# Kernel tuning notes

Measured on AMD Instinct MI355X. Metric: run time of the kernel, lower is better.

Reference implementation:

```python
import jax, jax.numpy as jnp
import numpy as np

N_JOINTS = 24

def _rodrigues(r):
    # r: [B, J, 3] axis-angle -> [B, J, 3, 3] rotation matrices
    theta = jnp.clip(jnp.linalg.norm(r, axis=-1, keepdims=True), 1e-6)  # [B,J,1]
    rh = r / theta
    z = jnp.zeros_like(rh[..., :1])
    # skew-symmetric matrix m
    m = jnp.stack([
        jnp.concatenate([z, -rh[..., 2:3], rh[..., 1:2]], -1),
        jnp.concatenate([rh[..., 2:3], z, -rh[..., 0:1]], -1),
        jnp.concatenate([-rh[..., 1:2], rh[..., 0:1], z], -1),
    ], axis=-2)  # [B,J,3,3]
    rrT = rh[..., :, None] * rh[..., None, :]  # outer product [B,J,3,3]
    cos = jnp.cos(theta)[..., None]
    sin = jnp.sin(theta)[..., None]
    eye = jnp.eye(3, dtype=r.dtype)
    return cos * eye + (1.0 - cos) * rrT + sin * m

def _with_zeros(Rm, t):
    # Rm: [B,3,3], t: [B,3] -> [B,4,4] homogeneous transform
    B = Rm.shape[0]
    top = jnp.concatenate([Rm, t[:, :, None]], axis=-1)  # [B,3,4]
    bot = jnp.broadcast_to(jnp.array([0.0, 0.0, 0.0, 1.0], Rm.dtype), (B, 1, 4))
    return jnp.concatenate([top, bot], axis=1)

def _keypoints(v, idx):
    # v: [B,N,3], idx: [G,K] vertex-index groups -> [B,G,3] via (max+min)/2
    g = v[:, idx]  # [B,G,K,3] irregular gather
    return (g.max(axis=2) + g.min(axis=2)) * 0.5

def setup_inputs() -> dict:
    key = jax.random.key(0)
    ks = jax.random.split(key, 8)
    B, N, P, K = 64, 40000, 100, 128
    beta = jax.random.normal(ks[0], (B, P), jnp.float32)
    pose = jax.random.normal(ks[1], (B, N_JOINTS * 3), jnp.float32) * 0.3
    trans = jax.random.normal(ks[2], (B, 3), jnp.float32)
    shapedirs = jax.random.normal(ks[3], (P, 3 * N), jnp.float32) * 0.01
    v_template = jax.random.normal(ks[4], (N, 3), jnp.float32)
    w = jax.random.uniform(ks[5], (N, N_JOINTS), jnp.float32)
    weights = w / w.sum(axis=1, keepdims=True)  # LBS weights sum to 1
    reorder_index = jnp.arange(N_JOINTS, dtype=jnp.int64 if jax.config.jax_enable_x64 else jnp.int32)
    # kinematic tree: parent[i] < i (binary-tree shape stands in for the rabbit skeleton)
    parent = jnp.concatenate([jnp.zeros(1, jnp.int32), (jnp.arange(1, N_JOINTS, dtype=jnp.int32) - 1) // 2])
    joint_idx = jax.random.randint(ks[6], (N_JOINTS - 1, K), 0, N)
    add_idx = jax.random.randint(ks[7], (7, K), 0, N)
    return {"beta": beta, "pose": pose, "trans": trans, "shapedirs": shapedirs,
            "v_template": v_template, "weights": weights, "reorder_index": reorder_index,
            "parent": parent, "joint_idx": joint_idx, "add_idx": add_idx}

def reference(beta, pose, trans, shapedirs, v_template, weights,
              reorder_index, parent, joint_idx, add_idx):
    B = beta.shape[0]
    pose = pose.reshape(B, N_JOINTS, 3)[:, reorder_index]
    # blend shapes: v_shaped = beta @ shapedirs + template
    v_posed = (beta @ shapedirs + v_template.reshape(-1)).reshape(B, -1, 3)  # [B,N,3]
    # joints from vertex-group (max+min)/2, root is zero
    J = jnp.concatenate([jnp.zeros((B, 1, 3), beta.dtype), _keypoints(v_posed, joint_idx)], axis=1)  # [B,24,3]
    R = _rodrigues(pose)  # [B,24,3,3]
    # forward kinematics along the tree (fixed 24-joint loop)
    par = np.asarray(jax.device_get(parent))
    G = [_with_zeros(R[:, 0], J[:, 0])]
    for i in range(1, N_JOINTS):
        p = int(par[i])
        G_loc = _with_zeros(R[:, i], J[:, i] - J[:, p])
        G.append(jnp.matmul(G[p], G_loc))
    G = jnp.stack(G, axis=1)  # [B,24,4,4]
    # remove rest-pose joint locations (pack subtraction only touches last column)
    Jh = jnp.concatenate([J, jnp.zeros((B, N_JOINTS, 1), beta.dtype)], axis=-1)[..., None]  # [B,24,4,1]
    t_corr = jnp.matmul(G, Jh)  # [B,24,4,1]
    G1 = jnp.concatenate([G[..., :3], G[..., 3:4] - t_corr], axis=-1)
    # LBS skinning: per-vertex blended transform
    T = jnp.einsum('nk,bkij->bnij', weights, G1)  # [B,N,4,4]
    vh = jnp.concatenate([v_posed, jnp.ones((B, v_posed.shape[1], 1), beta.dtype)], axis=-1)  # [B,N,4]
    posed = jnp.einsum('bnij,bnj->bni', T, vh)[..., :3] + trans[:, None, :]  # [B,N,3]
    skeleton = jnp.concatenate([
        jnp.zeros((B, 1, 3), beta.dtype),
        _keypoints(posed, joint_idx),
        _keypoints(posed, add_idx),
    ], axis=1)  # [B,31,3]
    return posed, skeleton
```

## Files before the change

### kernel.cpp

```cpp
#include <hip/hip_runtime.h>
#include <math.h>

#define B   64
#define NV  40000
#define P   100
#define KG  128
#define NJ  24
#define TV  16
#define NSK 31
#define NSUB (KG / TV)

typedef __attribute__((ext_vector_type(8))) short bf16x8;
typedef __attribute__((ext_vector_type(4))) float f32x4;

__device__ __forceinline__ unsigned short rne_bf16(float f) {
  unsigned u = __float_as_uint(f);
  u = (u + 0x7FFFu + ((u >> 16) & 1u)) >> 16;
  return (unsigned short)u;
}

__global__ __launch_bounds__(256)
void k_jpart(const float* __restrict__ beta,
             const float* __restrict__ sd,
             const float* __restrict__ vt,
             const int*   __restrict__ joint_idx,
             float*       __restrict__ pmn,
             float*       __restrict__ pmx) {
  const int j = blockIdx.x;
  const int s = blockIdx.y;
  const int t = threadIdx.x;
  const int lane = t & 63, wv = t >> 6;
  const int l15 = lane & 15, qd = lane >> 4;

  __shared__ __align__(16) unsigned short beta_s[64 * 136];
  __shared__ __align__(16) unsigned short sdT_s[48 * 136];
  __shared__ float vt_s[48];
  __shared__ int   idx_s[TV];
  float* pos_s = (float*)beta_s;

  if (t < TV) idx_s[t] = joint_idx[j * KG + s * TV + t];
  __syncthreads();

  for (int e = t; e < 64 * 36; e += 256) {
    const int m = e / 36, pp = P + e % 36;
    beta_s[m * 136 + pp] = 0;
  }
  for (int e = t; e < 64 * P; e += 256) {
    const int m = e / P, p = e % P;
    beta_s[m * 136 + p] = rne_bf16(beta[e]);
  }
  for (int task = t; task < 768; task += 256) {
    const int n = task % 48, kg = task / 48;
    const size_t colbase = (size_t)idx_s[n / 3] * 3 + (n % 3);
    unsigned pk[4];
#pragma unroll
    for (int h = 0; h < 4; ++h) {
      const int k0 = kg * 8 + 2 * h;
      float f0 = 0.0f, f1 = 0.0f;
      if (k0 < P)     f0 = sd[(size_t)k0 * (3 * NV) + colbase];
      if (k0 + 1 < P) f1 = sd[(size_t)(k0 + 1) * (3 * NV) + colbase];
      pk[h] = (unsigned)rne_bf16(f0) | ((unsigned)rne_bf16(f1) << 16);
    }
    *(uint4*)&sdT_s[n * 136 + kg * 8] = make_uint4(pk[0], pk[1], pk[2], pk[3]);
  }
  if (t < 48) vt_s[t] = vt[(size_t)idx_s[t / 3] * 3 + (t % 3)];
  __syncthreads();

  bf16x8 af[4];
#pragma unroll
  for (int ks = 0; ks < 4; ++ks)
    af[ks] = *(const bf16x8*)&beta_s[(wv * 16 + l15) * 136 + ks * 32 + qd * 8];
  f32x4 acc[3];
#pragma unroll
  for (int nt = 0; nt < 3; ++nt) acc[nt] = (f32x4){0.f, 0.f, 0.f, 0.f};
#pragma unroll
  for (int ks = 0; ks < 4; ++ks) {
#pragma unroll
    for (int nt = 0; nt < 3; ++nt) {
      const bf16x8 bf = *(const bf16x8*)&sdT_s[(nt * 16 + l15) * 136 + ks * 32 + qd * 8];
      acc[nt] = __builtin_amdgcn_mfma_f32_16x16x32_bf16(af[ks], bf, acc[nt], 0, 0, 0);
    }
  }
  float vtv[3];
#pragma unroll
  for (int nt = 0; nt < 3; ++nt) vtv[nt] = vt_s[nt * 16 + l15];
  __syncthreads();

#pragma unroll
  for (int nt = 0; nt < 3; ++nt) {
    const int n = nt * 16 + l15;
    const int v = n / 3, c = n - 3 * v;
#pragma unroll
    for (int r = 0; r < 4; ++r) {
      const int m = wv * 16 + qd * 4 + r;
      pos_s[m * 68 + v * 4 + c] = acc[nt][r] + vtv[nt];
    }
  }
  __syncthreads();

  if (t < 192) {
    const int b = t / 3, c = t % 3;
    float lo = 1e30f, hi = -1e30f;
#pragma unroll
    for (int v = 0; v < TV; ++v) {
      const float val = pos_s[b * 68 + v * 4 + c];
      lo = fminf(lo, val); hi = fmaxf(hi, val);
    }
    pmn[((j * NSUB + s) * B + b) * 3 + c] = lo;
    pmx[((j * NSUB + s) * B + b) * 3 + c] = hi;
  }
}

__global__ void k_chain(const float* __restrict__ pose,
                        const int*   __restrict__ parent,
                        const float* __restrict__ pmn,
                        const float* __restrict__ pmx,
                        const float* __restrict__ beta,
                        const float* __restrict__ trans,
                        unsigned short* __restrict__ G1A,
                        unsigned short* __restrict__ beta_bf) {
  const int b = blockIdx.x;
  const int t = threadIdx.x;

  __shared__ float R[NJ][9];
  __shared__ float Jl[NJ][3];
  __shared__ float G[NJ][12];
  __shared__ float G1c[NJ][12];

  if (t < NJ) {
    const float x = pose[b * NJ * 3 + t * 3 + 0];
    const float y = pose[b * NJ * 3 + t * 3 + 1];
    const float z = pose[b * NJ * 3 + t * 3 + 2];
    const float th = fmaxf(sqrtf(x * x + y * y + z * z), 1e-6f);
    const float xh = x / th, yh = y / th, zh = z / th;
    const float c = cosf(th), s = sinf(th), o = 1.0f - c;
    R[t][0] = c + o * xh * xh;      R[t][1] = o * xh * yh - s * zh; R[t][2] = o * xh * zh + s * yh;
    R[t][3] = o * xh * yh + s * zh; R[t][4] = c + o * yh * yh;      R[t][5] = o * yh * zh - s * xh;
    R[t][6] = o * xh * zh - s * yh; R[t][7] = o * yh * zh + s * xh; R[t][8] = c + o * zh * zh;
    if (t == 0) {
      Jl[0][0] = 0.0f; Jl[0][1] = 0.0f; Jl[0][2] = 0.0f;
    } else {
      const int jj = t - 1;
#pragma unroll
      for (int c2 = 0; c2 < 3; ++c2) {
        float lo = 1e30f, hi = -1e30f;
#pragma unroll
        for (int s2 = 0; s2 < NSUB; ++s2) {
          lo = fminf(lo, pmn[((jj * NSUB + s2) * B + b) * 3 + c2]);
          hi = fmaxf(hi, pmx[((jj * NSUB + s2) * B + b) * 3 + c2]);
        }
        Jl[t][c2] = 0.5f * (lo + hi);
      }
    }
  }
  __syncthreads();

  if (t < 12) {
    const int r = t >> 2, c = t & 3;
    G[0][t] = (c < 3) ? R[0][r * 3 + c] : Jl[0][r];
  }
  __syncthreads();

  for (int i = 1; i < NJ; ++i) {
    const int p = parent[i];
    if (t < 12) {
      const int r = t >> 2, c = t & 3;
      const float g0 = G[p][r * 4 + 0];
      const float g1 = G[p][r * 4 + 1];
      const float g2 = G[p][r * 4 + 2];
      float l0, l1, l2, add;
      if (c < 3) {
        l0 = R[i][0 * 3 + c]; l1 = R[i][1 * 3 + c]; l2 = R[i][2 * 3 + c];
        add = 0.0f;
      } else {
        l0 = Jl[i][0] - Jl[p][0]; l1 = Jl[i][1] - Jl[p][1]; l2 = Jl[i][2] - Jl[p][2];
        add = G[p][r * 4 + 3];
      }
      G[i][t] = g0 * l0 + g1 * l1 + g2 * l2 + add;
    }
    __syncthreads();
  }

  for (int e = t; e < NJ * 12; e += 64) {
    const int i = e / 12, rc = e % 12, r = rc >> 2, c = rc & 3;
    float val;
    if (c < 3) {
      val = G[i][rc];
    } else {
      val = G[i][r * 4 + 3] - (G[i][r * 4 + 0] * Jl[i][0] +
                               G[i][r * 4 + 1] * Jl[i][1] +
                               G[i][r * 4 + 2] * Jl[i][2]);
    }
    G1c[i][rc] = val;
  }
  __syncthreads();

  for (int e = t; e < 136; e += 64)
    beta_bf[b * 136 + e] = (e < P) ? rne_bf16(beta[b * P + e]) : (unsigned short)0;

  for (int e = t; e < 512; e += 64) {
    const int m = e >> 5, k = e & 31;
    float val = 0.0f;
    if (m < 12) {
      if (k < NJ) val = G1c[k][m];
      else if (k == NJ && (m & 3) == 3) val = trans[b * 3 + (m >> 2)];
    }
    G1A[(size_t)b * 512 + e] = rne_bf16(val);
  }
}

__global__ __launch_bounds__(256)
void k_skin(const float* __restrict__ sd,
            const float* __restrict__ vt,
            const float* __restrict__ w,
            const unsigned short* __restrict__ beta_bf,
            const unsigned short* __restrict__ G1A,
            float*       __restrict__ out) {
  const int n0v = blockIdx.x * TV;
  const int col0 = n0v * 3;
  const int t  = threadIdx.x;
  const int lane = t & 63, wv = t >> 6;
  const int l15 = lane & 15, q = lane >> 4;

  __shared__ __align__(16) unsigned short beta_s[64 * 136];
  __shared__ __align__(16) unsigned short sdT_s[48 * 136];
  __shared__ __align__(16) unsigned short wT_s[16 * 40];
  __shared__ float vt_s[48];
  float* vhf  = (float*)beta_s;
  float* pos_s = (float*)sdT_s;

  for (int e = t; e < 64 * 136 / 8; e += 256)
    ((uint4*)beta_s)[e] = ((const uint4*)beta_bf)[e];
  for (int task = t; task < 768; task += 256) {
    const int n = task % 48, kg = task / 48;
    unsigned pk[4];
#pragma unroll
    for (int h = 0; h < 4; ++h) {
      const int k0 = kg * 8 + 2 * h;
      float f0 = 0.0f, f1 = 0.0f;
      if (k0 < P)     f0 = sd[(size_t)k0 * (3 * NV) + col0 + n];
      if (k0 + 1 < P) f1 = sd[(size_t)(k0 + 1) * (3 * NV) + col0 + n];
      pk[h] = (unsigned)rne_bf16(f0) | ((unsigned)rne_bf16(f1) << 16);
    }
    *(uint4*)&sdT_s[n * 136 + kg * 8] = make_uint4(pk[0], pk[1], pk[2], pk[3]);
  }
  for (int e = t; e < 512; e += 256) {
    const int n = e >> 5, k = e & 31;
    float val = (k < NJ) ? w[(n0v + n) * NJ + k] : (k == NJ ? 1.0f : 0.0f);
    wT_s[n * 40 + k] = rne_bf16(val);
  }
  if (t < 48) vt_s[t] = vt[col0 + t];
  __syncthreads();

  bf16x8 af[4];
#pragma unroll
  for (int ks = 0; ks < 4; ++ks)
    af[ks] = *(const bf16x8*)&beta_s[(wv * 16 + l15) * 136 + ks * 32 + q * 8];
  f32x4 acc[3];
#pragma unroll
  for (int nt = 0; nt < 3; ++nt) acc[nt] = (f32x4){0.f, 0.f, 0.f, 0.f};
#pragma unroll
  for (int ks = 0; ks < 4; ++ks) {
#pragma unroll
    for (int nt = 0; nt < 3; ++nt) {
      const bf16x8 bf = *(const bf16x8*)&sdT_s[(nt * 16 + l15) * 136 + ks * 32 + q * 8];
      acc[nt] = __builtin_amdgcn_mfma_f32_16x16x32_bf16(af[ks], bf, acc[nt], 0, 0, 0);
    }
  }
  float vtv[3];
#pragma unroll
  for (int nt = 0; nt < 3; ++nt) vtv[nt] = vt_s[nt * 16 + l15];
  __syncthreads();

#pragma unroll
  for (int nt = 0; nt < 3; ++nt) {
    const int n = nt * 16 + l15;
    const int v = n / 3, c = n - 3 * v;
#pragma unroll
    for (int r = 0; r < 4; ++r) {
      const int m = wv * 16 + q * 4 + r;
      vhf[m * 68 + v * 4 + c] = acc[nt][r] + vtv[nt];
    }
  }
  __syncthreads();

  const bf16x8 wf = *(const bf16x8*)&wT_s[l15 * 40 + q * 8];
  const f32x4 zero = (f32x4){0.f, 0.f, 0.f, 0.f};
#pragma unroll 4
  for (int bi = 0; bi < 16; ++bi) {
    const int b = wv * 16 + bi;
    const bf16x8 gf = *(const bf16x8*)&G1A[(size_t)b * 512 + l15 * 32 + q * 8];
    const f32x4 d = __builtin_amdgcn_mfma_f32_16x16x32_bf16(gf, wf, zero, 0, 0, 0);
    const float4 vh = *(const float4*)&vhf[b * 68 + l15 * 4];
    if (q < 3) {
      const float pos = d[0] * vh.x + d[1] * vh.y + d[2] * vh.z + d[3];
      pos_s[b * 48 + l15 * 3 + q] = pos;
    }
  }
  __syncthreads();

  for (int e = t; e < 768; e += 256) {
    const int b = e / 12, ch = e % 12;
    const float4 val = *(const float4*)&pos_s[b * 48 + ch * 4];
    *(float4*)&out[(size_t)b * (NV * 3) + col0 + ch * 4] = val;
  }
}

__global__ void k_skel(const float* __restrict__ posed,
                       const int*   __restrict__ joint_idx,
                       const int*   __restrict__ add_idx,
                       float*       __restrict__ skel) {
  const int j = blockIdx.x;
  const int b = blockIdx.y;
  const int t = threadIdx.x;
  const int idx = (j < 23) ? joint_idx[j * KG + t] : add_idx[(j - 23) * KG + t];

  const float* p = posed + (size_t)b * NV * 3 + (size_t)idx * 3;
  float mn[3], mx[3];
#pragma unroll
  for (int c = 0; c < 3; ++c) { mn[c] = p[c]; mx[c] = p[c]; }
#pragma unroll
  for (int off = 32; off > 0; off >>= 1) {
#pragma unroll
    for (int c = 0; c < 3; ++c) {
      mn[c] = fminf(mn[c], __shfl_down(mn[c], off));
      mx[c] = fmaxf(mx[c], __shfl_down(mx[c], off));
    }
  }
  __shared__ float s_mn[2][3], s_mx[2][3];
  const int wave = t >> 6, lane = t & 63;
  if (lane == 0) {
#pragma unroll
    for (int c = 0; c < 3; ++c) { s_mn[wave][c] = mn[c]; s_mx[wave][c] = mx[c]; }
  }
  __syncthreads();
  if (t == 0) {
#pragma unroll
    for (int c = 0; c < 3; ++c) {
      float lo = fminf(s_mn[0][c], s_mn[1][c]);
      float hi = fmaxf(s_mx[0][c], s_mx[1][c]);
      skel[(b * NSK + 1 + j) * 3 + c] = 0.5f * (lo + hi);
      if (j == 0) skel[(b * NSK + 0) * 3 + c] = 0.0f;
    }
  }
}

extern "C" void kernel_launch(void* const* d_in, const int* in_sizes, int n_in,
                              void* d_out, int out_size, void* d_ws, size_t ws_size,
                              hipStream_t stream) {
  const float* beta     = (const float*)d_in[0];
  const float* pose     = (const float*)d_in[1];
  const float* trans    = (const float*)d_in[2];
  const float* sd       = (const float*)d_in[3];
  const float* vt       = (const float*)d_in[4];
  const float* w        = (const float*)d_in[5];
  const int* parent     = (const int*)d_in[7];
  const int* joint_idx  = (const int*)d_in[8];
  const int* add_idx    = (const int*)d_in[9];

  float* out = (float*)d_out;
  unsigned short* G1A     = (unsigned short*)d_ws;
  unsigned short* beta_bf = G1A + B * 512;
  float* pmn = (float*)(beta_bf + B * 136);
  float* pmx = pmn + 23 * NSUB * B * 3;

  k_jpart<<<dim3(23, NSUB), 256, 0, stream>>>(beta, sd, vt, joint_idx, pmn, pmx);
  k_chain<<<B, 64, 0, stream>>>(pose, parent, pmn, pmx, beta, trans, G1A, beta_bf);
  k_skin <<<NV / TV, 256, 0, stream>>>(sd, vt, w, beta_bf, G1A, out);
  k_skel <<<dim3(30, B), 128, 0, stream>>>(out, joint_idx, add_idx,
                                           out + (size_t)B * NV * 3);
}
```

Before: 158.0 us.

## Widen skinning tile to 32 vertices, write output directly, widen jpart blocks

The skinning kernel now processes 32 vertices per block instead of 16. The beta fragments loaded per block are reused across twice as many shapedirs columns, and the per-batch G1 fragment feeds two MFMAs. The LDS staging buffer for posed vertices is removed, and results are written straight to global memory as scalar stores, trading coalesced float4 writes for strided 4-byte stores. The joint-partial kernel is launched with 512 threads, and the extra waves only help with loading before sitting idle during the MFMA phase.

```diff
diff --git a/kernel.cpp b/kernel.cpp
--- a/kernel.cpp
+++ b/kernel.cpp
@@ -6,9 +6,10 @@
 #define P   100
 #define KG  128
 #define NJ  24
-#define TV  16
+#define TVJ 16
+#define TVS 32
 #define NSK 31
-#define NSUB (KG / TV)
+#define NSUB (KG / TVJ)
 
 typedef __attribute__((ext_vector_type(8))) short bf16x8;
 typedef __attribute__((ext_vector_type(4))) float f32x4;
@@ -19,7 +20,7 @@
   return (unsigned short)u;
 }
 
-__global__ __launch_bounds__(256)
+__global__ __launch_bounds__(512)
 void k_jpart(const float* __restrict__ beta,
              const float* __restrict__ sd,
              const float* __restrict__ vt,
@@ -35,21 +36,21 @@
   __shared__ __align__(16) unsigned short beta_s[64 * 136];
   __shared__ __align__(16) unsigned short sdT_s[48 * 136];
   __shared__ float vt_s[48];
-  __shared__ int   idx_s[TV];
+  __shared__ int   idx_s[TVJ];
   float* pos_s = (float*)beta_s;
 
-  if (t < TV) idx_s[t] = joint_idx[j * KG + s * TV + t];
-  __syncthreads();
-
-  for (int e = t; e < 64 * 36; e += 256) {
+  if (t < TVJ) idx_s[t] = joint_idx[j * KG + s * TVJ + t];
+  __syncthreads();
+
+  for (int e = t; e < 64 * 36; e += 512) {
     const int m = e / 36, pp = P + e % 36;
     beta_s[m * 136 + pp] = 0;
   }
-  for (int e = t; e < 64 * P; e += 256) {
+  for (int e = t; e < 64 * P; e += 512) {
     const int m = e / P, p = e % P;
     beta_s[m * 136 + p] = rne_bf16(beta[e]);
   }
-  for (int task = t; task < 768; task += 256) {
+  for (int task = t; task < 768; task += 512) {
     const int n = task % 48, kg = task / 48;
     const size_t colbase = (size_t)idx_s[n / 3] * 3 + (n % 3);
     unsigned pk[4];
@@ -66,34 +67,38 @@
   if (t < 48) vt_s[t] = vt[(size_t)idx_s[t / 3] * 3 + (t % 3)];
   __syncthreads();
 
-  bf16x8 af[4];
-#pragma unroll
-  for (int ks = 0; ks < 4; ++ks)
-    af[ks] = *(const bf16x8*)&beta_s[(wv * 16 + l15) * 136 + ks * 32 + qd * 8];
   f32x4 acc[3];
-#pragma unroll
-  for (int nt = 0; nt < 3; ++nt) acc[nt] = (f32x4){0.f, 0.f, 0.f, 0.f};
-#pragma unroll
-  for (int ks = 0; ks < 4; ++ks) {
+  float vtv[3];
+  if (wv < 4) {
+    bf16x8 af[4];
+#pragma unroll
+    for (int ks = 0; ks < 4; ++ks)
+      af[ks] = *(const bf16x8*)&beta_s[(wv * 16 + l15) * 136 + ks * 32 + qd * 8];
+#pragma unroll
+    for (int nt = 0; nt < 3; ++nt) acc[nt] = (f32x4){0.f, 0.f, 0.f, 0.f};
+#pragma unroll
+    for (int ks = 0; ks < 4; ++ks) {
+#pragma unroll
+      for (int nt = 0; nt < 3; ++nt) {
+        const bf16x8 bf = *(const bf16x8*)&sdT_s[(nt * 16 + l15) * 136 + ks * 32 + qd * 8];
+        acc[nt] = __builtin_amdgcn_mfma_f32_16x16x32_bf16(af[ks], bf, acc[nt], 0, 0, 0);
+      }
+    }
+#pragma unroll
+    for (int nt = 0; nt < 3; ++nt) vtv[nt] = vt_s[nt * 16 + l15];
+  }
+  __syncthreads();
+
+  if (wv < 4) {
 #pragma unroll
     for (int nt = 0; nt < 3; ++nt) {
-      const bf16x8 bf = *(const bf16x8*)&sdT_s[(nt * 16 + l15) * 136 + ks * 32 + qd * 8];
-      acc[nt] = __builtin_amdgcn_mfma_f32_16x16x32_bf16(af[ks], bf, acc[nt], 0, 0, 0);
-    }
-  }
-  float vtv[3];
-#pragma unroll
-  for (int nt = 0; nt < 3; ++nt) vtv[nt] = vt_s[nt * 16 + l15];
-  __syncthreads();
-
-#pragma unroll
-  for (int nt = 0; nt < 3; ++nt) {
-    const int n = nt * 16 + l15;
-    const int v = n / 3, c = n - 3 * v;
-#pragma unroll
-    for (int r = 0; r < 4; ++r) {
-      const int m = wv * 16 + qd * 4 + r;
-      pos_s[m * 68 + v * 4 + c] = acc[nt][r] + vtv[nt];
+      const int n = nt * 16 + l15;
+      const int v = n / 3, c = n - 3 * v;
+#pragma unroll
+      for (int r = 0; r < 4; ++r) {
+        const int m = wv * 16 + qd * 4 + r;
+        pos_s[m * 68 + v * 4 + c] = acc[nt][r] + vtv[nt];
+      }
     }
   }
   __syncthreads();
@@ -102,7 +107,7 @@
     const int b = t / 3, c = t % 3;
     float lo = 1e30f, hi = -1e30f;
 #pragma unroll
-    for (int v = 0; v < TV; ++v) {
+    for (int v = 0; v < TVJ; ++v) {
       const float val = pos_s[b * 68 + v * 4 + c];
       lo = fminf(lo, val); hi = fmaxf(hi, val);
     }
@@ -216,23 +221,23 @@
             const unsigned short* __restrict__ beta_bf,
             const unsigned short* __restrict__ G1A,
             float*       __restrict__ out) {
-  const int n0v = blockIdx.x * TV;
+  const int n0v  = blockIdx.x * TVS;
   const int col0 = n0v * 3;
   const int t  = threadIdx.x;
   const int lane = t & 63, wv = t >> 6;
   const int l15 = lane & 15, q = lane >> 4;
 
-  __shared__ __align__(16) unsigned short beta_s[64 * 136];
-  __shared__ __align__(16) unsigned short sdT_s[48 * 136];
-  __shared__ __align__(16) unsigned short wT_s[16 * 40];
-  __shared__ float vt_s[48];
-  float* vhf  = (float*)beta_s;
-  float* pos_s = (float*)sdT_s;
-
-  for (int e = t; e < 64 * 136 / 8; e += 256)
+  __shared__ __align__(16) unsigned char smem[46464];
+  unsigned short* beta_s = (unsigned short*)smem;
+  unsigned short* sdT_s  = (unsigned short*)(smem + 17408);
+  unsigned short* wT_s   = (unsigned short*)(smem + 43520);
+  float*          vt_s   = (float*)(smem + 46080);
+  float*          vhf    = (float*)smem;
+
+  for (int e = t; e < 1088; e += 256)
     ((uint4*)beta_s)[e] = ((const uint4*)beta_bf)[e];
-  for (int task = t; task < 768; task += 256) {
-    const int n = task % 48, kg = task / 48;
+  for (int task = t; task < 1536; task += 256) {
+    const int n = task % 96, kg = task / 96;
     unsigned pk[4];
 #pragma unroll
     for (int h = 0; h < 4; ++h) {
@@ -244,65 +249,61 @@
     }
     *(uint4*)&sdT_s[n * 136 + kg * 8] = make_uint4(pk[0], pk[1], pk[2], pk[3]);
   }
-  for (int e = t; e < 512; e += 256) {
+  for (int e = t; e < 1024; e += 256) {
     const int n = e >> 5, k = e & 31;
     float val = (k < NJ) ? w[(n0v + n) * NJ + k] : (k == NJ ? 1.0f : 0.0f);
     wT_s[n * 40 + k] = rne_bf16(val);
   }
-  if (t < 48) vt_s[t] = vt[col0 + t];
+  if (t < 96) vt_s[t] = vt[col0 + t];
   __syncthreads();
 
   bf16x8 af[4];
 #pragma unroll
   for (int ks = 0; ks < 4; ++ks)
     af[ks] = *(const bf16x8*)&beta_s[(wv * 16 + l15) * 136 + ks * 32 + q * 8];
-  f32x4 acc[3];
-#pragma unroll
-  for (int nt = 0; nt < 3; ++nt) acc[nt] = (f32x4){0.f, 0.f, 0.f, 0.f};
+  f32x4 acc[6];
+#pragma unroll
+  for (int nt = 0; nt < 6; ++nt) acc[nt] = (f32x4){0.f, 0.f, 0.f, 0.f};
 #pragma unroll
   for (int ks = 0; ks < 4; ++ks) {
 #pragma unroll
-    for (int nt = 0; nt < 3; ++nt) {
+    for (int nt = 0; nt < 6; ++nt) {
       const bf16x8 bf = *(const bf16x8*)&sdT_s[(nt * 16 + l15) * 136 + ks * 32 + q * 8];
       acc[nt] = __builtin_amdgcn_mfma_f32_16x16x32_bf16(af[ks], bf, acc[nt], 0, 0, 0);
     }
   }
-  float vtv[3];
-#pragma unroll
-  for (int nt = 0; nt < 3; ++nt) vtv[nt] = vt_s[nt * 16 + l15];
-  __syncthreads();
-
-#pragma unroll
-  for (int nt = 0; nt < 3; ++nt) {
+  __syncthreads();
+
+#pragma unroll
+  for (int nt = 0; nt < 6; ++nt) {
     const int n = nt * 16 + l15;
     const int v = n / 3, c = n - 3 * v;
+    const float vtn = vt_s[n];
 #pragma unroll
     for (int r = 0; r < 4; ++r) {
       const int m = wv * 16 + q * 4 + r;
-      vhf[m * 68 + v * 4 + c] = acc[nt][r] + vtv[nt];
-    }
-  }
-  __syncthreads();
-
-  const bf16x8 wf = *(const bf16x8*)&wT_s[l15 * 40 + q * 8];
+      vhf[m * 128 + v * 4 + c] = acc[nt][r] + vtn;
+    }
+  }
+  __syncthreads();
+
+  const bf16x8 wf0 = *(const bf16x8*)&wT_s[l15 * 40 + q * 8];
+  const bf16x8 wf1 = *(const bf16x8*)&wT_s[(16 + l15) * 40 + q * 8];
   const f32x4 zero = (f32x4){0.f, 0.f, 0.f, 0.f};
 #pragma unroll 4
   for (int bi = 0; bi < 16; ++bi) {
     const int b = wv * 16 + bi;
     const bf16x8 gf = *(const bf16x8*)&G1A[(size_t)b * 512 + l15 * 32 + q * 8];
-    const f32x4 d = __builtin_amdgcn_mfma_f32_16x16x32_bf16(gf, wf, zero, 0, 0, 0);
-    const float4 vh = *(const float4*)&vhf[b * 68 + l15 * 4];
+    const f32x4 d0 = __builtin_amdgcn_mfma_f32_16x16x32_bf16(gf, wf0, zero, 0, 0, 0);
+    const f32x4 d1 = __builtin_amdgcn_mfma_f32_16x16x32_bf16(gf, wf1, zero, 0, 0, 0);
+    const float4 vh0 = *(const float4*)&vhf[b * 128 + l15 * 4];
+    const float4 vh1 = *(const float4*)&vhf[b * 128 + 64 + l15 * 4];
     if (q < 3) {
-      const float pos = d[0] * vh.x + d[1] * vh.y + d[2] * vh.z + d[3];
-      pos_s[b * 48 + l15 * 3 + q] = pos;
-    }
-  }
-  __syncthreads();
-
-  for (int e = t; e < 768; e += 256) {
-    const int b = e / 12, ch = e % 12;
-    const float4 val = *(const float4*)&pos_s[b * 48 + ch * 4];
-    *(float4*)&out[(size_t)b * (NV * 3) + col0 + ch * 4] = val;
+      out[(size_t)b * (NV * 3) + col0 + l15 * 3 + q] =
+          d0[0] * vh0.x + d0[1] * vh0.y + d0[2] * vh0.z + d0[3];
+      out[(size_t)b * (NV * 3) + col0 + 48 + l15 * 3 + q] =
+          d1[0] * vh1.x + d1[1] * vh1.y + d1[2] * vh1.z + d1[3];
+    }
   }
 }
 
@@ -364,9 +365,9 @@
   float* pmn = (float*)(beta_bf + B * 136);
   float* pmx = pmn + 23 * NSUB * B * 3;
 
-  k_jpart<<<dim3(23, NSUB), 256, 0, stream>>>(beta, sd, vt, joint_idx, pmn, pmx);
+  k_jpart<<<dim3(23, NSUB), 512, 0, stream>>>(beta, sd, vt, joint_idx, pmn, pmx);
   k_chain<<<B, 64, 0, stream>>>(pose, parent, pmn, pmx, beta, trans, G1A, beta_bf);
-  k_skin <<<NV / TV, 256, 0, stream>>>(sd, vt, w, beta_bf, G1A, out);
+  k_skin <<<NV / TVS, 256, 0, stream>>>(sd, vt, w, beta_bf, G1A, out);
   k_skel <<<dim3(30, B), 128, 0, stream>>>(out, joint_idx, add_idx,
                                            out + (size_t)B * NV * 3);
 }
```

Result: no change. 160.2 us (+1.4%).
